# Kernel optimization log

Measured on AMD Instinct MI355X. Metric: run time of the kernel, lower is better.

The kernel has to match this reference:

```python
import jax, jax.numpy as jnp
import numpy as np

DIM = 64
SQRT_DIM = float(np.sqrt(DIM))


def setup_inputs() -> dict:
    rng = jax.random.key(0)
    k1, k2, k3, k4 = jax.random.split(rng, 4)
    B, S, D = 16, 2048, DIM
    query = jax.random.normal(k1, (B, S, D), dtype=jnp.float32)
    key = jax.random.normal(k2, (B, S, D), dtype=jnp.float32)
    value = jax.random.normal(k3, (B, S, D), dtype=jnp.float32)
    mask = jax.random.randint(k4, (B, S), 0, 2) == 1  # True = masked (pad)
    return {"query": query, "key": key, "value": value, "mask": mask}


def reference(query, key, value, mask):
    # score: [B, S, S]
    score = jnp.einsum('bsd,btd->bst', query, key) / SQRT_DIM
    # symmetric mask: position (i, j) masked if token i OR token j is padded
    m = jnp.logical_or(mask[:, :, None], mask[:, None, :])  # [B, S, S]
    score = jnp.where(m, -jnp.inf, score)
    attn = jax.nn.softmax(score, axis=-1)
    attn = jnp.where(m, 0.0, attn)
    context = jnp.einsum('bst,btd->bsd', attn, value)
    return (context, attn)
```

## Files before the change

### kernel.cpp

```cpp
#include <hip/hip_runtime.h>
#include <hip/hip_bf16.h>

#define NBATCH 16
#define SLEN   2048
#define DIM    64
#define TQ     64
#define NTHR   256
#define NW     4
#define PANEL  128
#define NPANEL (SLEN / PANEL)
#define PROWK  72
#define PROWV  136
#define PROWP  136

typedef __attribute__((ext_vector_type(8))) short bf16x8;
typedef __attribute__((ext_vector_type(4))) float f32x4;

__device__ inline short f2bf(float f) {
    union { __hip_bfloat16 h; short s; } u;
    u.h = __float2bfloat16(f);
    return u.s;
}
__device__ inline float bf2f(unsigned short s) {
    union { unsigned u; float f; } x;
    x.u = ((unsigned)s) << 16;
    return x.f;
}
__device__ inline bf16x8 pack8(float4 a, float4 b) {
    bf16x8 r;
    r[0] = f2bf(a.x); r[1] = f2bf(a.y); r[2] = f2bf(a.z); r[3] = f2bf(a.w);
    r[4] = f2bf(b.x); r[5] = f2bf(b.y); r[6] = f2bf(b.z); r[7] = f2bf(b.w);
    return r;
}

__global__ __launch_bounds__(NTHR, 3) void sdpa_kernel(
    const float* __restrict__ Q, const float* __restrict__ K,
    const float* __restrict__ V, const int* __restrict__ M,
    float* __restrict__ outCtx, float* __restrict__ outAttn)
{
    __shared__ __align__(16) short sK[128 * PROWK];
    __shared__ __align__(16) short sVT[64 * PROWV];
    __shared__ __align__(16) short sP[NW * 16 * PROWP];
    __shared__ float sMask[PANEL];

    const int tid = threadIdx.x;
    const int w = tid >> 6, l = tid & 63, g = l >> 4, c = l & 15;
    const int b  = blockIdx.x >> 5;
    const int i0 = (blockIdx.x & 31) * TQ;
    const int i0w = i0 + w * 16;

    const float* Kb = K + (size_t)b * SLEN * DIM;
    const float* Vb = V + (size_t)b * SLEN * DIM;
    const int*   Mb = M + b * SLEN;

    bf16x8 qa0, qa1;
    {
        const float* qp = Q + ((size_t)b * SLEN + i0w + c) * DIM + g * 8;
        qa0 = pack8(*(const float4*)(qp),      *(const float4*)(qp + 4));
        qa1 = pack8(*(const float4*)(qp + 32), *(const float4*)(qp + 36));
    }

    const float scl = 0.125f;
    float rsum[4] = {0.f, 0.f, 0.f, 0.f};

    for (int p = 0; p < NPANEL; p++) {
        const int j0 = p * PANEL;
        #pragma unroll
        for (int it = 0; it < 8; it++) {
            const int idx = it * NTHR + tid;
            const int row = idx >> 4, c4 = idx & 15;
            float4 kv = *(const float4*)(Kb + (size_t)(j0 + row) * DIM + c4 * 4);
            *(short4*)(sK + row * PROWK + c4 * 4) =
                make_short4(f2bf(kv.x), f2bf(kv.y), f2bf(kv.z), f2bf(kv.w));
        }
        if (tid < PANEL) sMask[tid] = Mb[j0 + tid] ? 0.f : 1.f;
        __syncthreads();
        #pragma unroll
        for (int jt = 0; jt < 8; jt++) {
            const short* kr = sK + (jt * 16 + c) * PROWK + g * 8;
            bf16x8 kb0 = *(const bf16x8*)(kr);
            bf16x8 kb1 = *(const bf16x8*)(kr + 32);
            f32x4 acc = {0.f, 0.f, 0.f, 0.f};
            acc = __builtin_amdgcn_mfma_f32_16x16x32_bf16(qa0, kb0, acc, 0, 0, 0);
            acc = __builtin_amdgcn_mfma_f32_16x16x32_bf16(qa1, kb1, acc, 0, 0, 0);
            const float em = sMask[jt * 16 + c];
            #pragma unroll
            for (int r = 0; r < 4; r++)
                rsum[r] += __expf(acc[r] * scl) * em;
        }
        __syncthreads();
    }
    #pragma unroll
    for (int off = 1; off < 16; off <<= 1) {
        #pragma unroll
        for (int r = 0; r < 4; r++)
            rsum[r] += __shfl_xor(rsum[r], off, 64);
    }
    float scv[4];
    #pragma unroll
    for (int r = 0; r < 4; r++) {
        const int rm = Mb[i0w + g * 4 + r];
        scv[r] = (rm || rsum[r] <= 0.f) ? 0.f : 1.f / rsum[r];
    }

    short* sPw = sP + w * 16 * PROWP;
    f32x4 pv[4];
    #pragma unroll
    for (int nt = 0; nt < 4; nt++) pv[nt] = (f32x4){0.f, 0.f, 0.f, 0.f};

    for (int p = 0; p < NPANEL; p++) {
        const int j0 = p * PANEL;
        #pragma unroll
        for (int it = 0; it < 8; it++) {
            const int idx = it * NTHR + tid;
            const int row = idx >> 4, c4 = idx & 15;
            float4 kv = *(const float4*)(Kb + (size_t)(j0 + row) * DIM + c4 * 4);
            *(short4*)(sK + row * PROWK + c4 * 4) =
                make_short4(f2bf(kv.x), f2bf(kv.y), f2bf(kv.z), f2bf(kv.w));
        }
        #pragma unroll
        for (int it = 0; it < 2; it++) {
            const int task = it * NTHR + tid;
            const int k4 = task >> 4, d4g = task & 15;
            const int kb = k4 * 4, d4 = d4g * 4;
            const int colb = kb ^ ((d4g & 3) << 3);
            const float* vp = Vb + (size_t)(j0 + kb) * DIM + d4;
            float4 r0 = *(const float4*)(vp);
            float4 r1 = *(const float4*)(vp + DIM);
            float4 r2 = *(const float4*)(vp + 2 * DIM);
            float4 r3 = *(const float4*)(vp + 3 * DIM);
            *(short4*)(sVT + (d4 + 0) * PROWV + colb) =
                make_short4(f2bf(r0.x), f2bf(r1.x), f2bf(r2.x), f2bf(r3.x));
            *(short4*)(sVT + (d4 + 1) * PROWV + colb) =
                make_short4(f2bf(r0.y), f2bf(r1.y), f2bf(r2.y), f2bf(r3.y));
            *(short4*)(sVT + (d4 + 2) * PROWV + colb) =
                make_short4(f2bf(r0.z), f2bf(r1.z), f2bf(r2.z), f2bf(r3.z));
            *(short4*)(sVT + (d4 + 3) * PROWV + colb) =
                make_short4(f2bf(r0.w), f2bf(r1.w), f2bf(r2.w), f2bf(r3.w));
        }
        if (tid < PANEL) sMask[tid] = Mb[j0 + tid] ? 0.f : 1.f;
        __syncthreads();

        #pragma unroll
        for (int jt = 0; jt < 8; jt++) {
            const short* kr = sK + (jt * 16 + c) * PROWK + g * 8;
            bf16x8 kb0 = *(const bf16x8*)(kr);
            bf16x8 kb1 = *(const bf16x8*)(kr + 32);
            f32x4 acc = {0.f, 0.f, 0.f, 0.f};
            acc = __builtin_amdgcn_mfma_f32_16x16x32_bf16(qa0, kb0, acc, 0, 0, 0);
            acc = __builtin_amdgcn_mfma_f32_16x16x32_bf16(qa1, kb1, acc, 0, 0, 0);
            const float em = sMask[jt * 16 + c];
            #pragma unroll
            for (int r = 0; r < 4; r++)
                sPw[(g * 4 + r) * PROWP + jt * 16 + c] =
                    f2bf(__expf(acc[r] * scl) * em * scv[r]);
        }

        #pragma unroll
        for (int ks = 0; ks < 4; ks++) {
            bf16x8 af = *(const bf16x8*)(sPw + c * PROWP + ks * 32 + g * 8);
            #pragma unroll
            for (int nt = 0; nt < 4; nt++) {
                const int d = nt * 16 + c;
                const int gp = g ^ ((d >> 2) & 3);
                bf16x8 bfrag = *(const bf16x8*)(sVT + d * PROWV + ks * 32 + gp * 8);
                pv[nt] = __builtin_amdgcn_mfma_f32_16x16x32_bf16(af, bfrag, pv[nt], 0, 0, 0);
            }
        }

        const size_t rowBase = (size_t)b * SLEN + i0w;
        #pragma unroll
        for (int it = 0; it < 8; it++) {
            const int idx = it * 64 + l;
            const int row = idx >> 5, col4 = idx & 31;
            const unsigned short* pp = (const unsigned short*)sPw + row * PROWP + col4 * 4;
            ushort4 p4 = *(const ushort4*)(pp);
            float4 o = {bf2f(p4.x), bf2f(p4.y), bf2f(p4.z), bf2f(p4.w)};
            *(float4*)(outAttn + (rowBase + row) * SLEN + j0 + col4 * 4) = o;
        }
        __syncthreads();
    }

    #pragma unroll
    for (int nt = 0; nt < 4; nt++) {
        #pragma unroll
        for (int r = 0; r < 4; r++)
            outCtx[((size_t)b * SLEN + i0w + g * 4 + r) * DIM + nt * 16 + c] = pv[nt][r];
    }
}

extern "C" void kernel_launch(void* const* d_in, const int* in_sizes, int n_in,
                              void* d_out, int out_size, void* d_ws, size_t ws_size,
                              hipStream_t stream) {
    const float* Q = (const float*)d_in[0];
    const float* K = (const float*)d_in[1];
    const float* V = (const float*)d_in[2];
    const int*   M = (const int*)d_in[3];
    float* outCtx  = (float*)d_out;
    float* outAttn = (float*)d_out + (size_t)NBATCH * SLEN * DIM;
    dim3 grid(NBATCH * (SLEN / TQ));
    sdpa_kernel<<<grid, NTHR, 0, stream>>>(Q, K, V, M, outCtx, outAttn);
}
```

Before: 374.9 us.

## Replace two-pass softmax with single pass, staging unnormalized bf16 probs in output

Removes the first pass over K that only computed row sums. Unnormalized exponentials are now accumulated into the row sum while P·V runs, and the context is scaled at the end. The unnormalized bf16 probabilities are parked in the upper half of each fp32 attention output row, then read back, scaled and expanded to fp32 in a final pass. This trades the QK recompute for extra global-memory traffic on the attention matrix. It also relies on exponentials not overflowing, since the row maximum is still not subtracted.

```diff
diff --git a/kernel.cpp b/kernel.cpp
--- a/kernel.cpp
+++ b/kernel.cpp
@@ -42,6 +42,7 @@
     __shared__ __align__(16) short sVT[64 * PROWV];
     __shared__ __align__(16) short sP[NW * 16 * PROWP];
     __shared__ float sMask[PANEL];
+    __shared__ float sScale[NW * 16];
 
     const int tid = threadIdx.x;
     const int w = tid >> 6, l = tid & 63, g = l >> 4, c = l & 15;
@@ -52,6 +53,7 @@
     const float* Kb = K + (size_t)b * SLEN * DIM;
     const float* Vb = V + (size_t)b * SLEN * DIM;
     const int*   Mb = M + b * SLEN;
+    float* win = outAttn + ((size_t)b * SLEN + i0w) * SLEN;
 
     bf16x8 qa0, qa1;
     {
@@ -62,51 +64,10 @@
 
     const float scl = 0.125f;
     float rsum[4] = {0.f, 0.f, 0.f, 0.f};
-
-    for (int p = 0; p < NPANEL; p++) {
-        const int j0 = p * PANEL;
-        #pragma unroll
-        for (int it = 0; it < 8; it++) {
-            const int idx = it * NTHR + tid;
-            const int row = idx >> 4, c4 = idx & 15;
-            float4 kv = *(const float4*)(Kb + (size_t)(j0 + row) * DIM + c4 * 4);
-            *(short4*)(sK + row * PROWK + c4 * 4) =
-                make_short4(f2bf(kv.x), f2bf(kv.y), f2bf(kv.z), f2bf(kv.w));
-        }
-        if (tid < PANEL) sMask[tid] = Mb[j0 + tid] ? 0.f : 1.f;
-        __syncthreads();
-        #pragma unroll
-        for (int jt = 0; jt < 8; jt++) {
-            const short* kr = sK + (jt * 16 + c) * PROWK + g * 8;
-            bf16x8 kb0 = *(const bf16x8*)(kr);
-            bf16x8 kb1 = *(const bf16x8*)(kr + 32);
-            f32x4 acc = {0.f, 0.f, 0.f, 0.f};
-            acc = __builtin_amdgcn_mfma_f32_16x16x32_bf16(qa0, kb0, acc, 0, 0, 0);
-            acc = __builtin_amdgcn_mfma_f32_16x16x32_bf16(qa1, kb1, acc, 0, 0, 0);
-            const float em = sMask[jt * 16 + c];
-            #pragma unroll
-            for (int r = 0; r < 4; r++)
-                rsum[r] += __expf(acc[r] * scl) * em;
-        }
-        __syncthreads();
-    }
-    #pragma unroll
-    for (int off = 1; off < 16; off <<= 1) {
-        #pragma unroll
-        for (int r = 0; r < 4; r++)
-            rsum[r] += __shfl_xor(rsum[r], off, 64);
-    }
-    float scv[4];
-    #pragma unroll
-    for (int r = 0; r < 4; r++) {
-        const int rm = Mb[i0w + g * 4 + r];
-        scv[r] = (rm || rsum[r] <= 0.f) ? 0.f : 1.f / rsum[r];
-    }
-
-    short* sPw = sP + w * 16 * PROWP;
     f32x4 pv[4];
     #pragma unroll
     for (int nt = 0; nt < 4; nt++) pv[nt] = (f32x4){0.f, 0.f, 0.f, 0.f};
+    short* sPw = sP + w * 16 * PROWP;
 
     for (int p = 0; p < NPANEL; p++) {
         const int j0 = p * PANEL;
@@ -151,9 +112,11 @@
             acc = __builtin_amdgcn_mfma_f32_16x16x32_bf16(qa1, kb1, acc, 0, 0, 0);
             const float em = sMask[jt * 16 + c];
             #pragma unroll
-            for (int r = 0; r < 4; r++)
-                sPw[(g * 4 + r) * PROWP + jt * 16 + c] =
-                    f2bf(__expf(acc[r] * scl) * em * scv[r]);
+            for (int r = 0; r < 4; r++) {
+                const float e = __expf(acc[r] * scl) * em;
+                rsum[r] += e;
+                sPw[(g * 4 + r) * PROWP + jt * 16 + c] = f2bf(e);
+            }
         }
 
         #pragma unroll
@@ -168,24 +131,57 @@
             }
         }
 
-        const size_t rowBase = (size_t)b * SLEN + i0w;
         #pragma unroll
         for (int it = 0; it < 8; it++) {
-            const int idx = it * 64 + l;
-            const int row = idx >> 5, col4 = idx & 31;
-            const unsigned short* pp = (const unsigned short*)sPw + row * PROWP + col4 * 4;
-            ushort4 p4 = *(const ushort4*)(pp);
-            float4 o = {bf2f(p4.x), bf2f(p4.y), bf2f(p4.z), bf2f(p4.w)};
-            *(float4*)(outAttn + (rowBase + row) * SLEN + j0 + col4 * 4) = o;
+            const int task = it * 64 + l;
+            const int row = task >> 5, c4 = task & 31;
+            short* dst = (short*)(win + (size_t)row * SLEN + SLEN / 2) + j0 + c4 * 4;
+            *(ushort4*)dst =
+                *(const ushort4*)((const unsigned short*)sPw + row * PROWP + c4 * 4);
         }
         __syncthreads();
+    }
+
+    #pragma unroll
+    for (int off = 1; off < 16; off <<= 1) {
+        #pragma unroll
+        for (int r = 0; r < 4; r++)
+            rsum[r] += __shfl_xor(rsum[r], off, 64);
+    }
+    float scv[4];
+    #pragma unroll
+    for (int r = 0; r < 4; r++) {
+        const int rm = Mb[i0w + g * 4 + r];
+        scv[r] = (rm || rsum[r] <= 0.f) ? 0.f : 1.f / rsum[r];
+    }
+    if (c == 0) {
+        #pragma unroll
+        for (int r = 0; r < 4; r++) sScale[w * 16 + g * 4 + r] = scv[r];
     }
 
     #pragma unroll
     for (int nt = 0; nt < 4; nt++) {
         #pragma unroll
         for (int r = 0; r < 4; r++)
-            outCtx[((size_t)b * SLEN + i0w + g * 4 + r) * DIM + nt * 16 + c] = pv[nt][r];
+            outCtx[((size_t)b * SLEN + i0w + g * 4 + r) * DIM + nt * 16 + c] =
+                pv[nt][r] * scv[r];
+    }
+
+    for (int row = 0; row < 16; row++) {
+        const unsigned short* srow =
+            (const unsigned short*)(win + (size_t)row * SLEN + SLEN / 2);
+        const float sc = sScale[w * 16 + row];
+        ushort4 d[8];
+        #pragma unroll
+        for (int it = 0; it < 8; it++)
+            d[it] = *(const ushort4*)(srow + it * 256 + l * 4);
+        asm volatile("" ::: "memory");
+        #pragma unroll
+        for (int it = 0; it < 8; it++) {
+            float4 o = {bf2f(d[it].x) * sc, bf2f(d[it].y) * sc,
+                        bf2f(d[it].z) * sc, bf2f(d[it].w) * sc};
+            *(float4*)(win + (size_t)row * SLEN + it * 256 + l * 4) = o;
+        }
     }
 }
 
```

Measured after the change: 396.8 us. 1.06x slower.

## Fuse row-sum into PV pass, feed P to MFMA from registers, write attn in final pass

Applied to the files above, without the earlier changes.

Reorders the kernel into one pass that computes unnormalized exp scores, accumulates the row sums and multiplies by V in a single sweep, applying normalization to the context at the end. A second pass recomputes the scores to write normalized attention directly from registers as float4 stores. Swapping the MFMA operands puts the P fragment in register layout, so it goes straight into f16 16x16x16 MFMAs without staging through shared memory. The per-wave P buffer is gone and the occupancy hint rises to 4. The trade-offs are fp16 precision for P and V, and overflow risk in the unnormalized exp values.

```diff
diff --git a/kernel.cpp b/kernel.cpp
--- a/kernel.cpp
+++ b/kernel.cpp
@@ -6,25 +6,19 @@
 #define DIM    64
 #define TQ     64
 #define NTHR   256
-#define NW     4
 #define PANEL  128
 #define NPANEL (SLEN / PANEL)
 #define PROWK  72
-#define PROWV  136
-#define PROWP  136
+#define PROWV  134
 
 typedef __attribute__((ext_vector_type(8))) short bf16x8;
 typedef __attribute__((ext_vector_type(4))) float f32x4;
+typedef __attribute__((ext_vector_type(4))) _Float16 f16x4;
 
 __device__ inline short f2bf(float f) {
     union { __hip_bfloat16 h; short s; } u;
     u.h = __float2bfloat16(f);
     return u.s;
-}
-__device__ inline float bf2f(unsigned short s) {
-    union { unsigned u; float f; } x;
-    x.u = ((unsigned)s) << 16;
-    return x.f;
 }
 __device__ inline bf16x8 pack8(float4 a, float4 b) {
     bf16x8 r;
@@ -33,21 +27,19 @@
     return r;
 }
 
-__global__ __launch_bounds__(NTHR, 3) void sdpa_kernel(
+__global__ __launch_bounds__(NTHR, 4) void sdpa_kernel(
     const float* __restrict__ Q, const float* __restrict__ K,
     const float* __restrict__ V, const int* __restrict__ M,
     float* __restrict__ outCtx, float* __restrict__ outAttn)
 {
-    __shared__ __align__(16) short sK[128 * PROWK];
-    __shared__ __align__(16) short sVT[64 * PROWV];
-    __shared__ __align__(16) short sP[NW * 16 * PROWP];
+    __shared__ __align__(16) short sK[PANEL * PROWK];
+    __shared__ __align__(16) _Float16 sVT[DIM * PROWV];
     __shared__ float sMask[PANEL];
 
     const int tid = threadIdx.x;
     const int w = tid >> 6, l = tid & 63, g = l >> 4, c = l & 15;
     const int b  = blockIdx.x >> 5;
-    const int i0 = (blockIdx.x & 31) * TQ;
-    const int i0w = i0 + w * 16;
+    const int i0w = (blockIdx.x & 31) * TQ + w * 16;
 
     const float* Kb = K + (size_t)b * SLEN * DIM;
     const float* Vb = V + (size_t)b * SLEN * DIM;
@@ -59,51 +51,10 @@
         qa0 = pack8(*(const float4*)(qp),      *(const float4*)(qp + 4));
         qa1 = pack8(*(const float4*)(qp + 32), *(const float4*)(qp + 36));
     }
+    const int rowm = Mb[i0w + c];
 
     const float scl = 0.125f;
-    float rsum[4] = {0.f, 0.f, 0.f, 0.f};
-
-    for (int p = 0; p < NPANEL; p++) {
-        const int j0 = p * PANEL;
-        #pragma unroll
-        for (int it = 0; it < 8; it++) {
-            const int idx = it * NTHR + tid;
-            const int row = idx >> 4, c4 = idx & 15;
-            float4 kv = *(const float4*)(Kb + (size_t)(j0 + row) * DIM + c4 * 4);
-            *(short4*)(sK + row * PROWK + c4 * 4) =
-                make_short4(f2bf(kv.x), f2bf(kv.y), f2bf(kv.z), f2bf(kv.w));
-        }
-        if (tid < PANEL) sMask[tid] = Mb[j0 + tid] ? 0.f : 1.f;
-        __syncthreads();
-        #pragma unroll
-        for (int jt = 0; jt < 8; jt++) {
-            const short* kr = sK + (jt * 16 + c) * PROWK + g * 8;
-            bf16x8 kb0 = *(const bf16x8*)(kr);
-            bf16x8 kb1 = *(const bf16x8*)(kr + 32);
-            f32x4 acc = {0.f, 0.f, 0.f, 0.f};
-            acc = __builtin_amdgcn_mfma_f32_16x16x32_bf16(qa0, kb0, acc, 0, 0, 0);
-            acc = __builtin_amdgcn_mfma_f32_16x16x32_bf16(qa1, kb1, acc, 0, 0, 0);
-            const float em = sMask[jt * 16 + c];
-            #pragma unroll
-            for (int r = 0; r < 4; r++)
-                rsum[r] += __expf(acc[r] * scl) * em;
-        }
-        __syncthreads();
-    }
-    #pragma unroll
-    for (int off = 1; off < 16; off <<= 1) {
-        #pragma unroll
-        for (int r = 0; r < 4; r++)
-            rsum[r] += __shfl_xor(rsum[r], off, 64);
-    }
-    float scv[4];
-    #pragma unroll
-    for (int r = 0; r < 4; r++) {
-        const int rm = Mb[i0w + g * 4 + r];
-        scv[r] = (rm || rsum[r] <= 0.f) ? 0.f : 1.f / rsum[r];
-    }
-
-    short* sPw = sP + w * 16 * PROWP;
+    float rsum0 = 0.f, rsum1 = 0.f, rsum2 = 0.f, rsum3 = 0.f;
     f32x4 pv[4];
     #pragma unroll
     for (int nt = 0; nt < 4; nt++) pv[nt] = (f32x4){0.f, 0.f, 0.f, 0.f};
@@ -121,22 +72,21 @@
         #pragma unroll
         for (int it = 0; it < 2; it++) {
             const int task = it * NTHR + tid;
-            const int k4 = task >> 4, d4g = task & 15;
-            const int kb = k4 * 4, d4 = d4g * 4;
-            const int colb = kb ^ ((d4g & 3) << 3);
+            const int kb = (task >> 4) * 4, d4 = (task & 15) * 4;
             const float* vp = Vb + (size_t)(j0 + kb) * DIM + d4;
             float4 r0 = *(const float4*)(vp);
             float4 r1 = *(const float4*)(vp + DIM);
             float4 r2 = *(const float4*)(vp + 2 * DIM);
             float4 r3 = *(const float4*)(vp + 3 * DIM);
-            *(short4*)(sVT + (d4 + 0) * PROWV + colb) =
-                make_short4(f2bf(r0.x), f2bf(r1.x), f2bf(r2.x), f2bf(r3.x));
-            *(short4*)(sVT + (d4 + 1) * PROWV + colb) =
-                make_short4(f2bf(r0.y), f2bf(r1.y), f2bf(r2.y), f2bf(r3.y));
-            *(short4*)(sVT + (d4 + 2) * PROWV + colb) =
-                make_short4(f2bf(r0.z), f2bf(r1.z), f2bf(r2.z), f2bf(r3.z));
-            *(short4*)(sVT + (d4 + 3) * PROWV + colb) =
-                make_short4(f2bf(r0.w), f2bf(r1.w), f2bf(r2.w), f2bf(r3.w));
+            f16x4 t;
+            t[0] = (_Float16)r0.x; t[1] = (_Float16)r1.x; t[2] = (_Float16)r2.x; t[3] = (_Float16)r3.x;
+            *(f16x4*)(sVT + (d4 + 0) * PROWV + kb) = t;
+            t[0] = (_Float16)r0.y; t[1] = (_Float16)r1.y; t[2] = (_Float16)r2.y; t[3] = (_Float16)r3.y;
+            *(f16x4*)(sVT + (d4 + 1) * PROWV + kb) = t;
+            t[0] = (_Float16)r0.z; t[1] = (_Float16)r1.z; t[2] = (_Float16)r2.z; t[3] = (_Float16)r3.z;
+            *(f16x4*)(sVT + (d4 + 2) * PROWV + kb) = t;
+            t[0] = (_Float16)r0.w; t[1] = (_Float16)r1.w; t[2] = (_Float16)r2.w; t[3] = (_Float16)r3.w;
+            *(f16x4*)(sVT + (d4 + 3) * PROWV + kb) = t;
         }
         if (tid < PANEL) sMask[tid] = Mb[j0 + tid] ? 0.f : 1.f;
         __syncthreads();
@@ -147,45 +97,72 @@
             bf16x8 kb0 = *(const bf16x8*)(kr);
             bf16x8 kb1 = *(const bf16x8*)(kr + 32);
             f32x4 acc = {0.f, 0.f, 0.f, 0.f};
-            acc = __builtin_amdgcn_mfma_f32_16x16x32_bf16(qa0, kb0, acc, 0, 0, 0);
-            acc = __builtin_amdgcn_mfma_f32_16x16x32_bf16(qa1, kb1, acc, 0, 0, 0);
-            const float em = sMask[jt * 16 + c];
-            #pragma unroll
-            for (int r = 0; r < 4; r++)
-                sPw[(g * 4 + r) * PROWP + jt * 16 + c] =
-                    f2bf(__expf(acc[r] * scl) * em * scv[r]);
-        }
-
-        #pragma unroll
-        for (int ks = 0; ks < 4; ks++) {
-            bf16x8 af = *(const bf16x8*)(sPw + c * PROWP + ks * 32 + g * 8);
+            acc = __builtin_amdgcn_mfma_f32_16x16x32_bf16(kb0, qa0, acc, 0, 0, 0);
+            acc = __builtin_amdgcn_mfma_f32_16x16x32_bf16(kb1, qa1, acc, 0, 0, 0);
+            const float4 mv = *(const float4*)(sMask + jt * 16 + g * 4);
+            const float e0 = __expf(acc[0] * scl) * mv.x;
+            const float e1 = __expf(acc[1] * scl) * mv.y;
+            const float e2 = __expf(acc[2] * scl) * mv.z;
+            const float e3 = __expf(acc[3] * scl) * mv.w;
+            rsum0 += e0; rsum1 += e1; rsum2 += e2; rsum3 += e3;
+            f16x4 pfrag;
+            pfrag[0] = (_Float16)e0; pfrag[1] = (_Float16)e1;
+            pfrag[2] = (_Float16)e2; pfrag[3] = (_Float16)e3;
+            const _Float16* vb = sVT + jt * 16 + g * 4;
             #pragma unroll
             for (int nt = 0; nt < 4; nt++) {
-                const int d = nt * 16 + c;
-                const int gp = g ^ ((d >> 2) & 3);
-                bf16x8 bfrag = *(const bf16x8*)(sVT + d * PROWV + ks * 32 + gp * 8);
-                pv[nt] = __builtin_amdgcn_mfma_f32_16x16x32_bf16(af, bfrag, pv[nt], 0, 0, 0);
+                f16x4 vfrag = *(const f16x4*)(vb + (nt * 16 + c) * PROWV);
+                pv[nt] = __builtin_amdgcn_mfma_f32_16x16x16f16(pfrag, vfrag, pv[nt], 0, 0, 0);
             }
-        }
-
-        const size_t rowBase = (size_t)b * SLEN + i0w;
-        #pragma unroll
-        for (int it = 0; it < 8; it++) {
-            const int idx = it * 64 + l;
-            const int row = idx >> 5, col4 = idx & 31;
-            const unsigned short* pp = (const unsigned short*)sPw + row * PROWP + col4 * 4;
-            ushort4 p4 = *(const ushort4*)(pp);
-            float4 o = {bf2f(p4.x), bf2f(p4.y), bf2f(p4.z), bf2f(p4.w)};
-            *(float4*)(outAttn + (rowBase + row) * SLEN + j0 + col4 * 4) = o;
         }
         __syncthreads();
     }
 
+    float s = rsum0 + rsum1 + rsum2 + rsum3;
+    s += __shfl_xor(s, 16, 64);
+    s += __shfl_xor(s, 32, 64);
+    const float scv = (rowm || s <= 0.f) ? 0.f : 1.f / s;
+
     #pragma unroll
-    for (int nt = 0; nt < 4; nt++) {
+    for (int r = 0; r < 4; r++) {
+        const float scr = __shfl(scv, g * 4 + r, 64);
         #pragma unroll
-        for (int r = 0; r < 4; r++)
-            outCtx[((size_t)b * SLEN + i0w + g * 4 + r) * DIM + nt * 16 + c] = pv[nt][r];
+        for (int nt = 0; nt < 4; nt++)
+            outCtx[((size_t)b * SLEN + i0w + g * 4 + r) * DIM + nt * 16 + c] =
+                pv[nt][r] * scr;
+    }
+
+    float* arow = outAttn + ((size_t)b * SLEN + i0w + c) * SLEN;
+    for (int p = 0; p < NPANEL; p++) {
+        const int j0 = p * PANEL;
+        #pragma unroll
+        for (int it = 0; it < 8; it++) {
+            const int idx = it * NTHR + tid;
+            const int row = idx >> 4, c4 = idx & 15;
+            float4 kv = *(const float4*)(Kb + (size_t)(j0 + row) * DIM + c4 * 4);
+            *(short4*)(sK + row * PROWK + c4 * 4) =
+                make_short4(f2bf(kv.x), f2bf(kv.y), f2bf(kv.z), f2bf(kv.w));
+        }
+        if (tid < PANEL) sMask[tid] = Mb[j0 + tid] ? 0.f : 1.f;
+        __syncthreads();
+
+        #pragma unroll
+        for (int jt = 0; jt < 8; jt++) {
+            const short* kr = sK + (jt * 16 + c) * PROWK + g * 8;
+            bf16x8 kb0 = *(const bf16x8*)(kr);
+            bf16x8 kb1 = *(const bf16x8*)(kr + 32);
+            f32x4 acc = {0.f, 0.f, 0.f, 0.f};
+            acc = __builtin_amdgcn_mfma_f32_16x16x32_bf16(kb0, qa0, acc, 0, 0, 0);
+            acc = __builtin_amdgcn_mfma_f32_16x16x32_bf16(kb1, qa1, acc, 0, 0, 0);
+            const float4 mv = *(const float4*)(sMask + jt * 16 + g * 4);
+            float4 o;
+            o.x = __expf(acc[0] * scl) * mv.x * scv;
+            o.y = __expf(acc[1] * scl) * mv.y * scv;
+            o.z = __expf(acc[2] * scl) * mv.z * scv;
+            o.w = __expf(acc[3] * scl) * mv.w * scv;
+            *(float4*)(arow + j0 + jt * 16 + g * 4) = o;
+        }
+        __syncthreads();
     }
 }
 
```

New measurement: 485.1 us. +29.4%, slower.
